# Optimization experiments

Hardware: AMD Instinct MI355X
Metric: run time of the kernel (lower is better)

Reference implementation:

```python
import jax, jax.numpy as jnp
import numpy as np

B, T, C, H = 4, 4096, 2048, 128  # batch, seq, emb_dim, head_size


def setup_inputs() -> dict:
    key = jax.random.key(0)
    k1, k2, k3, k4 = jax.random.split(key, 4)
    idx = jax.random.normal(k1, (B, T, C), dtype=jnp.float32)
    # nn.Linear weight layout: [out_features, in_features]; scale like torch init
    s = 1.0 / np.sqrt(C)
    Wq = jax.random.uniform(k2, (H, C), jnp.float32, -s, s)
    Wk = jax.random.uniform(k3, (H, C), jnp.float32, -s, s)
    Wv = jax.random.uniform(k4, (H, C), jnp.float32, -s, s)
    return {"idx": idx, "Wq": Wq, "Wk": Wk, "Wv": Wv}


def reference(idx, Wq, Wk, Wv):
    b, t, c = idx.shape
    q = jnp.einsum('btc,hc->bth', idx, Wq)  # [B,T,H]
    k = jnp.einsum('btc,hc->bth', idx, Wk)
    v = jnp.einsum('btc,hc->bth', idx, Wv)
    # NOTE: original computes keys @ queries^T and scales by emb_dim**-0.5
    scale = jnp.asarray(c, idx.dtype) ** -0.5
    wei = jnp.einsum('bih,bjh->bij', k, q) * scale  # [B,T,T]
    causal = jnp.tril(jnp.ones((t, t), dtype=bool))
    wei = jnp.where(causal, wei, -jnp.inf)
    wei = jax.nn.softmax(wei, axis=-1)
    return jnp.einsum('bij,bjh->bih', wei, v)  # [B,T,H]
```

## Files before the change

### kernel.cpp

```cpp
#include <hip/hip_runtime.h>
#include <hip/hip_bf16.h>
#include <cstdint>

#define TSEQ 4096
#define CDIM 2048
#define HDIM 128

typedef short bf8v __attribute__((ext_vector_type(8)));
typedef float f4v  __attribute__((ext_vector_type(4)));

__device__ __forceinline__ unsigned short f2b(float f) {
  union { float f; unsigned u; } v; v.f = f;
  unsigned u = v.u;
  return (unsigned short)((u + 0x7fffu + ((u >> 16) & 1u)) >> 16);
}

__device__ __forceinline__ f4v mfma16(bf8v a, bf8v b, f4v c) {
  return __builtin_amdgcn_mfma_f32_16x16x32_bf16(a, b, c, 0, 0, 0);
}

__global__ void wcat_kernel(const float* __restrict__ Wq, const float* __restrict__ Wk,
                            const float* __restrict__ Wv, unsigned short* __restrict__ Wcat) {
  int c = blockIdx.x * 256 + threadIdx.x;
  int lane = c & 63;
  int kkg  = (c >> 6) & 63;
  int nb   = c >> 12;
  int n  = nb * 16 + (lane & 15);
  int k0 = kkg * 32 + (lane >> 4) * 8;
  const float* src;
  if (n < 128)      src = Wq + (size_t)n * CDIM + k0;
  else if (n < 256) src = Wk + (size_t)(n - 128) * CDIM + k0;
  else              src = Wv + (size_t)(n - 256) * CDIM + k0;
  float4 f0 = ((const float4*)src)[0];
  float4 f1 = ((const float4*)src)[1];
  bf8v o;
  o[0] = (short)f2b(f0.x); o[1] = (short)f2b(f0.y);
  o[2] = (short)f2b(f0.z); o[3] = (short)f2b(f0.w);
  o[4] = (short)f2b(f1.x); o[5] = (short)f2b(f1.y);
  o[6] = (short)f2b(f1.z); o[7] = (short)f2b(f1.w);
  *(bf8v*)(Wcat + (size_t)c * 8) = o;
}

__global__ __launch_bounds__(512, 2) void proj_gemm(const float* __restrict__ A,
                                                    const unsigned short* __restrict__ Bw,
                                                    unsigned short* __restrict__ QB,
                                                    unsigned short* __restrict__ KA,
                                                    unsigned short* __restrict__ VB) {
  __shared__ unsigned short Ct[64][392];
  const int m0 = blockIdx.x * 64;
  const int tid = threadIdx.x;
  const int lane = tid & 63;
  const int w = tid >> 6;
  const int sub = w & 3;
  const int cg  = w >> 2;
  const int llo = lane & 15, lhi = lane >> 4;

  f4v acc[12];
#pragma unroll
  for (int j = 0; j < 12; ++j) acc[j] = (f4v){0.f, 0.f, 0.f, 0.f};

  const float* ap = A + (size_t)(m0 + sub * 16 + llo) * CDIM + lhi * 8;

  float4 fa00 = *(const float4*)(ap);
  float4 fa01 = *(const float4*)(ap + 4);
  float4 fa10 = *(const float4*)(ap + 32);
  float4 fa11 = *(const float4*)(ap + 36);

  const unsigned short* bbase = Bw + (size_t)(cg * 12) * 64 * 64 * 8 + (size_t)lane * 8;

  for (int it = 0; it < 32; ++it) {
    bf8v af[2];
    af[0][0] = (short)f2b(fa00.x); af[0][1] = (short)f2b(fa00.y);
    af[0][2] = (short)f2b(fa00.z); af[0][3] = (short)f2b(fa00.w);
    af[0][4] = (short)f2b(fa01.x); af[0][5] = (short)f2b(fa01.y);
    af[0][6] = (short)f2b(fa01.z); af[0][7] = (short)f2b(fa01.w);
    af[1][0] = (short)f2b(fa10.x); af[1][1] = (short)f2b(fa10.y);
    af[1][2] = (short)f2b(fa10.z); af[1][3] = (short)f2b(fa10.w);
    af[1][4] = (short)f2b(fa11.x); af[1][5] = (short)f2b(fa11.y);
    af[1][6] = (short)f2b(fa11.z); af[1][7] = (short)f2b(fa11.w);
    if (it < 31) {
      const float* apn = ap + (it + 1) * 64;
      fa00 = *(const float4*)(apn);
      fa01 = *(const float4*)(apn + 4);
      fa10 = *(const float4*)(apn + 32);
      fa11 = *(const float4*)(apn + 36);
    }
#pragma unroll
    for (int kk = 0; kk < 2; ++kk) {
      const int kkg = it * 2 + kk;
      bf8v bf[12];
#pragma unroll
      for (int j = 0; j < 12; ++j)
        bf[j] = *(const bf8v*)(bbase + ((size_t)j * 64 + kkg) * 64 * 8);
#pragma unroll
      for (int j = 0; j < 12; ++j) acc[j] = mfma16(af[kk], bf[j], acc[j]);
    }
  }

#pragma unroll
  for (int j = 0; j < 12; ++j)
#pragma unroll
    for (int r = 0; r < 4; ++r)
      Ct[sub * 16 + lhi * 4 + r][cg * 192 + j * 16 + llo] = f2b(acc[j][r]);
  __syncthreads();

  {
    const size_t base16 = (size_t)(m0 >> 4);
#pragma unroll
    for (int yy = 0; yy < 2; ++yy) {
      unsigned short* dst = yy ? KA : QB;
      const int colb = yy * 128;
#pragma unroll
      for (int p = 0; p < 2; ++p) {
        int g = p * 512 + tid;
        int t16l = g >> 8, kk2 = (g >> 6) & 3, ln = g & 63;
        int lo = ln & 15, hi = ln >> 4;
        bf8v v = *(const bf8v*)&Ct[t16l * 16 + lo][colb + kk2 * 32 + hi * 8];
        *(bf8v*)(dst + (((base16 + t16l) * 4 + kk2) * 64 + ln) * 8) = v;
      }
    }
  }
  {
    const size_t base32 = (size_t)(m0 >> 5);
#pragma unroll
    for (int p = 0; p < 3; ++p) {
      int g = p * 512 + tid;
      if (g < 1152) {
        int jbl = g / 576;
        int ht  = (g % 576) >> 6;
        int ln  = g & 63;
        int lo = ln & 15, hi = ln >> 4;
        bf8v v;
        if (ht == 8) {
#pragma unroll
          for (int e = 0; e < 8; ++e) v[e] = (lo == 0) ? (short)0x3F80 : (short)0;
        } else {
#pragma unroll
          for (int e = 0; e < 8; ++e) v[e] = (short)Ct[jbl * 32 + hi * 8 + e][256 + ht * 16 + lo];
        }
        *(bf8v*)(VB + (((base32 + jbl) * 9 + ht) * 512 + (size_t)ln * 8)) = v;
      }
    }
  }
}

__global__ __launch_bounds__(256, 4) void attn6(const unsigned short* __restrict__ QB,
                                                const unsigned short* __restrict__ KA,
                                                const unsigned short* __restrict__ VB,
                                                float* __restrict__ out) {
  __shared__ union SM {
    unsigned short Ps[4][2][16][68];
    struct { float Om[4][16][68]; float Lm[4][16]; } mg;
  } sm;
  const int x = blockIdx.x;
  const int b = x & 3;
  const int u = x >> 2;
  const int g = u >> 6, r0 = u & 63;
  const int s = (g & 1) ? (g * 64 + 63 - r0) : (g * 64 + r0);
  const int lastjt = s >> 2;
  const int tid = threadIdx.x;
  const int w = tid >> 6, lane = tid & 63;
  const int llo = lane & 15, lhi = lane >> 4;
  const float scale = 0.022097086912079608f;

  bf8v aK[4];
  {
    const unsigned short* kp = KA + (size_t)(b * 256 + s) * 2048;
#pragma unroll
    for (int kk = 0; kk < 4; ++kk) aK[kk] = *(const bf8v*)(kp + (kk * 64 + lane) * 8);
  }

  f4v Oacc[9];
#pragma unroll
  for (int nt = 0; nt < 9; ++nt) Oacc[nt] = (f4v){0.f, 0.f, 0.f, 0.f};

  auto computeS = [&](int jtS, int buf) {
    const unsigned short* qp = QB + (size_t)(b * 256 + jtS * 4) * 2048;
#pragma unroll
    for (int ct = 0; ct < 4; ++ct) {
      f4v acc = (f4v){0.f, 0.f, 0.f, 0.f};
#pragma unroll
      for (int kk = 0; kk < 4; ++kk) {
        bf8v bq = *(const bf8v*)(qp + ((ct * 4 + kk) * 64 + lane) * 8);
        acc = mfma16(aK[kk], bq, acc);
      }
#pragma unroll
      for (int r = 0; r < 4; ++r) {
        float sv = acc[r];
        if (jtS == lastjt) {
          int j = jtS * 64 + ct * 16 + llo;
          int i = s * 16 + lhi * 4 + r;
          if (j > i) sv = -3.0e38f;
        }
        sm.Ps[w][buf][lhi * 4 + r][ct * 16 + llo] = f2b(__expf(sv * scale));
      }
    }
  };

  if (w <= lastjt) computeS(w, 0);
  int buf = 0;
  for (int jt = w; jt <= lastjt; jt += 4) {
    bf8v aP0 = *(const bf8v*)&sm.Ps[w][buf][llo][lhi * 8];
    bf8v aP1 = *(const bf8v*)&sm.Ps[w][buf][llo][32 + lhi * 8];
    if (jt + 4 <= lastjt) computeS(jt + 4, buf ^ 1);
    const unsigned short* vp = VB + (size_t)(b * 128 + jt * 2) * 4608;
#pragma unroll
    for (int nt = 0; nt < 9; ++nt) {
      f4v o = Oacc[nt];
      o = mfma16(aP0, *(const bf8v*)(vp + nt * 512 + (size_t)lane * 8), o);
      o = mfma16(aP1, *(const bf8v*)(vp + 4608 + nt * 512 + (size_t)lane * 8), o);
      Oacc[nt] = o;
    }
    buf ^= 1;
  }

#pragma unroll
  for (int half = 0; half < 2; ++half) {
    __syncthreads();
#pragma unroll
    for (int nt = 0; nt < 4; ++nt)
#pragma unroll
      for (int r = 0; r < 4; ++r)
        sm.mg.Om[w][lhi * 4 + r][nt * 16 + llo] = Oacc[half * 4 + nt][r];
    if (half == 0 && llo == 0) {
#pragma unroll
      for (int r = 0; r < 4; ++r) sm.mg.Lm[w][lhi * 4 + r] = Oacc[8][r];
    }
    __syncthreads();
    {
      int row = tid >> 4, c0 = (tid & 15) * 4;
      float L = sm.mg.Lm[0][row] + sm.mg.Lm[1][row] + sm.mg.Lm[2][row] + sm.mg.Lm[3][row];
      float inv = 1.0f / L;
      float* op = out + (size_t)(b * TSEQ + s * 16 + row) * HDIM + half * 64 + c0;
#pragma unroll
      for (int e = 0; e < 4; ++e) {
        float o = sm.mg.Om[0][row][c0 + e] + sm.mg.Om[1][row][c0 + e] +
                  sm.mg.Om[2][row][c0 + e] + sm.mg.Om[3][row][c0 + e];
        op[e] = o * inv;
      }
    }
  }
}

extern "C" void kernel_launch(void* const* d_in, const int* in_sizes, int n_in,
                              void* d_out, int out_size, void* d_ws, size_t ws_size,
                              hipStream_t stream) {
  const float* idx = (const float*)d_in[0];
  const float* Wq  = (const float*)d_in[1];
  const float* Wk  = (const float*)d_in[2];
  const float* Wv  = (const float*)d_in[3];
  float* out = (float*)d_out;
  char* ws = (char*)d_ws;
  unsigned short* Wcat = (unsigned short*)ws;
  unsigned short* QB   = (unsigned short*)(ws + ((size_t)2  << 20));
  unsigned short* KA   = (unsigned short*)(ws + ((size_t)7  << 20));
  unsigned short* VB   = (unsigned short*)(ws + ((size_t)12 << 20));

  wcat_kernel<<<384, 256, 0, stream>>>(Wq, Wk, Wv, Wcat);
  proj_gemm<<<256, 512, 0, stream>>>(idx, Wcat, QB, KA, VB);
  attn6<<<1024, 256, 0, stream>>>(QB, KA, VB, out);
}
```

Measured before the change: 337.2 us.

## Restructure projection GEMM with async LDS A-staging and 3-way output split

The projection GEMM is split across a second grid dimension so each block computes one of Q/K/V (128 columns) with 256 threads instead of all 384 columns with 512 threads. Activations are staged into a swizzled triple-buffered LDS ring via global_load_lds, and B fragments are software-prefetched one step ahead. A packed bf16 conversion instruction replaces the scalar rounding. This aims for more blocks in flight and better latency hiding in the memory-bound fp32 input read. The cost is that each activation tile is now read three times from global memory (once per grid y), relying on L2 to absorb the reuse.

```diff
diff --git a/kernel.cpp b/kernel.cpp
--- a/kernel.cpp
+++ b/kernel.cpp
@@ -15,8 +15,20 @@
   return (unsigned short)((u + 0x7fffu + ((u >> 16) & 1u)) >> 16);
 }
 
+__device__ __forceinline__ unsigned cvtpk(float a, float b) {
+  unsigned r;
+  asm("v_cvt_pk_bf16_f32 %0, %1, %2" : "=v"(r) : "v"(a), "v"(b));
+  return r;
+}
+
 __device__ __forceinline__ f4v mfma16(bf8v a, bf8v b, f4v c) {
   return __builtin_amdgcn_mfma_f32_16x16x32_bf16(a, b, c, 0, 0, 0);
+}
+
+__device__ __forceinline__ void gload_lds16(const void* g, void* l) {
+  __builtin_amdgcn_global_load_lds(
+      (const __attribute__((address_space(1))) unsigned int*)g,
+      (__attribute__((address_space(3))) unsigned int*)l, 16, 0, 0);
 }
 
 __global__ void wcat_kernel(const float* __restrict__ Wq, const float* __restrict__ Wk,
@@ -41,90 +53,108 @@
   *(bf8v*)(Wcat + (size_t)c * 8) = o;
 }
 
-__global__ __launch_bounds__(512, 2) void proj_gemm(const float* __restrict__ A,
+__global__ __launch_bounds__(256, 4) void proj_gemm(const float* __restrict__ A,
                                                     const unsigned short* __restrict__ Bw,
                                                     unsigned short* __restrict__ QB,
                                                     unsigned short* __restrict__ KA,
                                                     unsigned short* __restrict__ VB) {
-  __shared__ unsigned short Ct[64][392];
+  __shared__ union {
+    float As[3][64][32];
+    unsigned short Ct[64][132];
+  } sm;
   const int m0 = blockIdx.x * 64;
+  const int y  = blockIdx.y;
   const int tid = threadIdx.x;
   const int lane = tid & 63;
   const int w = tid >> 6;
-  const int sub = w & 3;
-  const int cg  = w >> 2;
+  const int wm = (w & 1) * 32;
+  const int wn = (w >> 1) * 64;
   const int llo = lane & 15, lhi = lane >> 4;
 
-  f4v acc[12];
-#pragma unroll
-  for (int j = 0; j < 12; ++j) acc[j] = (f4v){0.f, 0.f, 0.f, 0.f};
-
-  const float* ap = A + (size_t)(m0 + sub * 16 + llo) * CDIM + lhi * 8;
-
-  float4 fa00 = *(const float4*)(ap);
-  float4 fa01 = *(const float4*)(ap + 4);
-  float4 fa10 = *(const float4*)(ap + 32);
-  float4 fa11 = *(const float4*)(ap + 36);
-
-  const unsigned short* bbase = Bw + (size_t)(cg * 12) * 64 * 64 * 8 + (size_t)lane * 8;
-
-  for (int it = 0; it < 32; ++it) {
+  f4v acc[2][4];
+#pragma unroll
+  for (int i = 0; i < 2; ++i)
+#pragma unroll
+    for (int j = 0; j < 4; ++j) acc[i][j] = (f4v){0.f, 0.f, 0.f, 0.f};
+
+  const int ar8 = lane >> 3;
+  const int agr = (lane & 7) ^ ar8;
+  const float* aptr = A + (size_t)(m0 + w * 16 + ar8) * CDIM + agr * 4;
+  auto stageA = [&](int it, int buf) {
+#pragma unroll
+    for (int q = 0; q < 2; ++q)
+      gload_lds16(aptr + (size_t)q * 8 * CDIM + it * 32, &sm.As[buf][w * 16 + q * 8][0]);
+  };
+
+  const unsigned short* bptr =
+      Bw + (size_t)(y * 8 + (w >> 1) * 4) * 64 * 512 + (size_t)lane * 8;
+  auto loadB = [&](bf8v* dst, int it) {
+#pragma unroll
+    for (int j = 0; j < 4; ++j)
+      dst[j] = *(const bf8v*)(bptr + (size_t)(j * 64 + it) * 512);
+  };
+
+  stageA(0, 0);
+  stageA(1, 1);
+  bf8v bcur[4];
+  loadB(bcur, 0);
+
+  int rb = 0;
+  for (int it = 0; it < 64; ++it) {
+    asm volatile("s_waitcnt vmcnt(6)" ::: "memory");
+    __builtin_amdgcn_s_barrier();
+    __builtin_amdgcn_sched_barrier(0);
+    if (it < 62) {
+      int wb = rb + 2; if (wb >= 3) wb -= 3;
+      stageA(it + 2, wb);
+    }
+    bf8v bnxt[4];
+    if (it < 63) loadB(bnxt, it + 1);
     bf8v af[2];
-    af[0][0] = (short)f2b(fa00.x); af[0][1] = (short)f2b(fa00.y);
-    af[0][2] = (short)f2b(fa00.z); af[0][3] = (short)f2b(fa00.w);
-    af[0][4] = (short)f2b(fa01.x); af[0][5] = (short)f2b(fa01.y);
-    af[0][6] = (short)f2b(fa01.z); af[0][7] = (short)f2b(fa01.w);
-    af[1][0] = (short)f2b(fa10.x); af[1][1] = (short)f2b(fa10.y);
-    af[1][2] = (short)f2b(fa10.z); af[1][3] = (short)f2b(fa10.w);
-    af[1][4] = (short)f2b(fa11.x); af[1][5] = (short)f2b(fa11.y);
-    af[1][6] = (short)f2b(fa11.z); af[1][7] = (short)f2b(fa11.w);
-    if (it < 31) {
-      const float* apn = ap + (it + 1) * 64;
-      fa00 = *(const float4*)(apn);
-      fa01 = *(const float4*)(apn + 4);
-      fa10 = *(const float4*)(apn + 32);
-      fa11 = *(const float4*)(apn + 36);
-    }
-#pragma unroll
-    for (int kk = 0; kk < 2; ++kk) {
-      const int kkg = it * 2 + kk;
-      bf8v bf[12];
-#pragma unroll
-      for (int j = 0; j < 12; ++j)
-        bf[j] = *(const bf8v*)(bbase + ((size_t)j * 64 + kkg) * 64 * 8);
-#pragma unroll
-      for (int j = 0; j < 12; ++j) acc[j] = mfma16(af[kk], bf[j], acc[j]);
-    }
-  }
-
-#pragma unroll
-  for (int j = 0; j < 12; ++j)
-#pragma unroll
-    for (int r = 0; r < 4; ++r)
-      Ct[sub * 16 + lhi * 4 + r][cg * 192 + j * 16 + llo] = f2b(acc[j][r]);
+#pragma unroll
+    for (int i = 0; i < 2; ++i) {
+      const float* ab = &sm.As[rb][wm + i * 16 + llo][0];
+      float4 f0 = *(const float4*)(ab + (((lhi << 1) | 0) ^ (llo & 7)) * 4);
+      float4 f1 = *(const float4*)(ab + (((lhi << 1) | 1) ^ (llo & 7)) * 4);
+      union { bf8v v; unsigned u[4]; } o;
+      o.u[0] = cvtpk(f0.x, f0.y); o.u[1] = cvtpk(f0.z, f0.w);
+      o.u[2] = cvtpk(f1.x, f1.y); o.u[3] = cvtpk(f1.z, f1.w);
+      af[i] = o.v;
+    }
+#pragma unroll
+    for (int i = 0; i < 2; ++i)
+#pragma unroll
+      for (int j = 0; j < 4; ++j) acc[i][j] = mfma16(af[i], bcur[j], acc[i][j]);
+#pragma unroll
+    for (int j = 0; j < 4; ++j) bcur[j] = bnxt[j];
+    rb = (rb == 2) ? 0 : rb + 1;
+  }
+
   __syncthreads();
-
-  {
+#pragma unroll
+  for (int i = 0; i < 2; ++i)
+#pragma unroll
+    for (int j = 0; j < 4; ++j)
+#pragma unroll
+      for (int r = 0; r < 4; ++r)
+        sm.Ct[wm + i * 16 + lhi * 4 + r][wn + j * 16 + llo] = f2b(acc[i][j][r]);
+  __syncthreads();
+  if (y < 2) {
+    unsigned short* dst = (y == 0) ? QB : KA;
     const size_t base16 = (size_t)(m0 >> 4);
 #pragma unroll
-    for (int yy = 0; yy < 2; ++yy) {
-      unsigned short* dst = yy ? KA : QB;
-      const int colb = yy * 128;
-#pragma unroll
-      for (int p = 0; p < 2; ++p) {
-        int g = p * 512 + tid;
-        int t16l = g >> 8, kk2 = (g >> 6) & 3, ln = g & 63;
-        int lo = ln & 15, hi = ln >> 4;
-        bf8v v = *(const bf8v*)&Ct[t16l * 16 + lo][colb + kk2 * 32 + hi * 8];
-        *(bf8v*)(dst + (((base16 + t16l) * 4 + kk2) * 64 + ln) * 8) = v;
-      }
-    }
-  }
-  {
+    for (int p = 0; p < 4; ++p) {
+      int g = p * 256 + tid;
+      int t16l = g >> 8, kk = (g >> 6) & 3, ln = g & 63;
+      int lo = ln & 15, hi = ln >> 4;
+      bf8v v = *(const bf8v*)&sm.Ct[t16l * 16 + lo][kk * 32 + hi * 8];
+      *(bf8v*)(dst + (((base16 + t16l) * 4 + kk) * 64 + ln) * 8) = v;
+    }
+  } else {
     const size_t base32 = (size_t)(m0 >> 5);
 #pragma unroll
-    for (int p = 0; p < 3; ++p) {
-      int g = p * 512 + tid;
+    for (int p = 0; p < 5; ++p) {
+      int g = p * 256 + tid;
       if (g < 1152) {
         int jbl = g / 576;
         int ht  = (g % 576) >> 6;
@@ -136,7 +166,7 @@
           for (int e = 0; e < 8; ++e) v[e] = (lo == 0) ? (short)0x3F80 : (short)0;
         } else {
 #pragma unroll
-          for (int e = 0; e < 8; ++e) v[e] = (short)Ct[jbl * 32 + hi * 8 + e][256 + ht * 16 + lo];
+          for (int e = 0; e < 8; ++e) v[e] = (short)sm.Ct[jbl * 32 + hi * 8 + e][ht * 16 + lo];
         }
         *(bf8v*)(VB + (((base32 + jbl) * 9 + ht) * 512 + (size_t)ln * 8)) = v;
       }
@@ -257,6 +287,6 @@
   unsigned short* VB   = (unsigned short*)(ws + ((size_t)12 << 20));
 
   wcat_kernel<<<384, 256, 0, stream>>>(Wq, Wk, Wv, Wcat);
-  proj_gemm<<<256, 512, 0, stream>>>(idx, Wcat, QB, KA, VB);
+  proj_gemm<<<dim3(256, 3), 256, 0, stream>>>(idx, Wcat, QB, KA, VB);
   attn6<<<1024, 256, 0, stream>>>(QB, KA, VB, out);
 }
```

After: 305.5 us. 9.4% less time.
